# Kernel optimization log

Measured on AMD Instinct MI355X. Metric: run time of the kernel, lower is better.

Reference implementation:

```python
import jax, jax.numpy as jnp
import numpy as np

EPS_LN = 1e-5  # nn.LayerNorm default eps
EPS_AD = 1e-5  # AdaIN calc_mean_std eps


def calc_mean_std(feat):
    # feat: [B, S, D]; instance-norm style stats per channel over the seq axis
    mean = jnp.mean(feat, axis=1, keepdims=True)
    var = jnp.var(feat, axis=1, keepdims=True, ddof=1)  # torch .var() is unbiased
    return mean, jnp.sqrt(var + EPS_AD)


def adain(content, style):
    c_mean, c_std = calc_mean_std(content)
    s_mean, s_std = calc_mean_std(style)
    return (content - c_mean) / c_std * s_std + s_mean


def layernorm(x, g, b):
    mu = jnp.mean(x, axis=-1, keepdims=True)
    var = jnp.mean(jnp.square(x - mu), axis=-1, keepdims=True)
    return (x - mu) * jax.lax.rsqrt(var + EPS_LN) * g + b


def silu(x):
    return x * jax.nn.sigmoid(x)


def setup_inputs() -> dict:
    B, S, D = 64, 256, 1024
    key = jax.random.key(0)
    ks = jax.random.split(key, 8)
    sc = lambda n: 1.0 / np.sqrt(n)
    return {
        "x": jax.random.normal(ks[0], (B, S, 2 * D), jnp.float32),
        "embed": jax.random.normal(ks[1], (B, S, D), jnp.float32),
        "style_code": jax.random.normal(ks[2], (B, S, D), jnp.float32),
        # conct: Linear(2*dim, dim)
        "Wc": jax.random.normal(ks[3], (D, 2 * D), jnp.float32) * sc(2 * D),
        "bc": jnp.zeros((D,), jnp.float32),
        # emb_fc: Linear(dim, dim)
        "We": jax.random.normal(ks[4], (D, D), jnp.float32) * sc(D),
        "be": jnp.zeros((D,), jnp.float32),
        # fc0: Conv1d(seq0, seq1, 1) -> [seq1, seq0] matrix over the seq axis
        "W0": jax.random.normal(ks[5], (S, S), jnp.float32) * sc(S),
        "b0": jnp.zeros((S,), jnp.float32),
        # fc1: Linear(dim, dim)
        "W1": jax.random.normal(ks[6], (D, D), jnp.float32) * sc(D),
        "b1": jnp.zeros((D,), jnp.float32),
        # LayerNorm affine params
        "g0": jnp.ones((D,), jnp.float32),
        "beta0": jnp.zeros((D,), jnp.float32),
        "g1": jnp.ones((D,), jnp.float32),
        "beta1": jnp.zeros((D,), jnp.float32),
    }


def reference(x, embed, style_code, Wc, bc, We, be, W0, b0, W1, b1, g0, beta0, g1, beta1):
    # conct (first=True): [B,S,2D] -> [B,S,D]
    adain_input = jnp.einsum('bse,de->bsd', x, Wc) + bc
    tmp = adain(adain_input, style_code)  # alpha = 1.0 so tmp replaces adain_input
    x = tmp + (jnp.einsum('bsd,ed->bse', silu(embed), We) + be)
    # block 0: LN -> 1x1 Conv1d over seq axis -> SiLU -> residual
    x_ = layernorm(x, g0, beta0)
    x_ = jnp.einsum('ts,bsd->btd', W0, x_) + b0[:, None]
    x = x + silu(x_)
    # block 1: LN -> Linear over dim axis -> SiLU -> residual
    x_ = layernorm(x, g1, beta1)
    x_ = jnp.einsum('bsd,ed->bse', x_, W1) + b1
    x = x + silu(x_)
    return (x, embed, style_code)
```

## Files before the change

kernel.cpp:

```cpp
#include <hip/hip_runtime.h>
#include <cstddef>

#define BB 64
#define SS 256
#define DD 1024
#define MM (BB * SS)

typedef unsigned short u16;
typedef short bf16x8 __attribute__((ext_vector_type(8)));
typedef float f32x4 __attribute__((ext_vector_type(4)));

#define LDSTRIDE 40

__device__ __forceinline__ float silu_f(float v) {
    return v * (1.0f / (1.0f + __expf(-v)));
}

__device__ __forceinline__ void split2(float f0, float f1, unsigned& hp, unsigned& lp) {
    const unsigned b0 = __float_as_uint(f0), b1 = __float_as_uint(f1);
    const unsigned h0 = b0 & 0xFFFF0000u, h1 = b1 & 0xFFFF0000u;
    const float l0 = f0 - __uint_as_float(h0);
    const float l1 = f1 - __uint_as_float(h1);
    hp = (h0 >> 16) | h1;
    lp = (__float_as_uint(l0) >> 16) | (__float_as_uint(l1) & 0xFFFF0000u);
}

template<bool SILU_A, int EPI>
__global__ __launch_bounds__(256, 2)
void gemm_nt_mfma(const float* __restrict__ A, const float* __restrict__ Bw,
                  const float* __restrict__ bias,
                  const float* __restrict__ t0, const float* __restrict__ scl,
                  const float* __restrict__ shf, const float* __restrict__ resid,
                  float* __restrict__ C, int M, int N, int K)
{
    __shared__ u16 lds[4 * 128 * LDSTRIDE];
    u16* Ah = lds;
    u16* Al = lds + 128 * LDSTRIDE;
    u16* Bh = lds + 2 * 128 * LDSTRIDE;
    u16* Bl = lds + 3 * 128 * LDSTRIDE;

    const int nbx = gridDim.x;
    const int nwg = nbx * gridDim.y;
    int lin = blockIdx.y * nbx + blockIdx.x;
    if ((nwg & 7) == 0) {
        const int cpx = nwg >> 3;
        lin = (lin & 7) * cpx + (lin >> 3);
    }
    const int bx = lin % nbx;
    const int by = lin / nbx;
    const int row0 = by * 128;
    const int col0 = bx * 128;

    const int tid  = threadIdx.x;
    const int srow = tid >> 1;
    const int sko  = (tid & 1) << 4;
    const int wbase = srow * LDSTRIDE + sko;

    const float* Ag = A  + (size_t)(row0 + srow) * K + sko;
    const float* Bg = Bw + (size_t)(col0 + srow) * K + sko;

    const int lane = tid & 63;
    const int wid  = tid >> 6;
    const int wr = wid >> 1, wc = wid & 1;
    const int fr = lane & 15;
    const int fh = lane >> 4;
    const int abase = (wr * 64 + fr) * LDSTRIDE + fh * 8;
    const int bbase = (wc * 64 + fr) * LDSTRIDE + fh * 8;

    f32x4 acc[4][4];
    const f32x4 zero = {0.f, 0.f, 0.f, 0.f};
#pragma unroll
    for (int i = 0; i < 4; ++i)
#pragma unroll
        for (int j = 0; j < 4; ++j) acc[i][j] = zero;

    for (int k0 = 0; k0 < K; k0 += 32) {
        float4 va[4], vb[4];
#pragma unroll
        for (int q = 0; q < 4; ++q) va[q] = *(const float4*)(Ag + k0 + q * 4);
#pragma unroll
        for (int q = 0; q < 4; ++q) vb[q] = *(const float4*)(Bg + k0 + q * 4);
        if (SILU_A) {
#pragma unroll
            for (int q = 0; q < 4; ++q) {
                va[q].x = silu_f(va[q].x); va[q].y = silu_f(va[q].y);
                va[q].z = silu_f(va[q].z); va[q].w = silu_f(va[q].w);
            }
        }
        uint4 ah0, al0, ah1, al1, bh0, bl0, bh1, bl1;
        split2(va[0].x, va[0].y, ah0.x, al0.x); split2(va[0].z, va[0].w, ah0.y, al0.y);
        split2(va[1].x, va[1].y, ah0.z, al0.z); split2(va[1].z, va[1].w, ah0.w, al0.w);
        split2(va[2].x, va[2].y, ah1.x, al1.x); split2(va[2].z, va[2].w, ah1.y, al1.y);
        split2(va[3].x, va[3].y, ah1.z, al1.z); split2(va[3].z, va[3].w, ah1.w, al1.w);
        split2(vb[0].x, vb[0].y, bh0.x, bl0.x); split2(vb[0].z, vb[0].w, bh0.y, bl0.y);
        split2(vb[1].x, vb[1].y, bh0.z, bl0.z); split2(vb[1].z, vb[1].w, bh0.w, bl0.w);
        split2(vb[2].x, vb[2].y, bh1.x, bl1.x); split2(vb[2].z, vb[2].w, bh1.y, bl1.y);
        split2(vb[3].x, vb[3].y, bh1.z, bl1.z); split2(vb[3].z, vb[3].w, bh1.w, bl1.w);

        __syncthreads();
        *(uint4*)&Ah[wbase] = ah0;  *(uint4*)&Ah[wbase + 8] = ah1;
        *(uint4*)&Al[wbase] = al0;  *(uint4*)&Al[wbase + 8] = al1;
        *(uint4*)&Bh[wbase] = bh0;  *(uint4*)&Bh[wbase + 8] = bh1;
        *(uint4*)&Bl[wbase] = bl0;  *(uint4*)&Bl[wbase + 8] = bl1;
        __syncthreads();

        bf16x8 fah[4], fal[4];
#pragma unroll
        for (int i = 0; i < 4; ++i) {
            fah[i] = *(const bf16x8*)&Ah[abase + i * 16 * LDSTRIDE];
            fal[i] = *(const bf16x8*)&Al[abase + i * 16 * LDSTRIDE];
        }
#pragma unroll
        for (int j = 0; j < 4; ++j) {
            const bf16x8 fbh = *(const bf16x8*)&Bh[bbase + j * 16 * LDSTRIDE];
            const bf16x8 fbl = *(const bf16x8*)&Bl[bbase + j * 16 * LDSTRIDE];
#pragma unroll
            for (int i = 0; i < 4; ++i) {
                acc[i][j] = __builtin_amdgcn_mfma_f32_16x16x32_bf16(fah[i], fbh, acc[i][j], 0, 0, 0);
                acc[i][j] = __builtin_amdgcn_mfma_f32_16x16x32_bf16(fal[i], fbh, acc[i][j], 0, 0, 0);
                acc[i][j] = __builtin_amdgcn_mfma_f32_16x16x32_bf16(fah[i], fbl, acc[i][j], 0, 0, 0);
            }
        }
    }

#pragma unroll
    for (int i = 0; i < 4; ++i) {
        const int rbase = row0 + wr * 64 + i * 16 + fh * 4;
#pragma unroll
        for (int j = 0; j < 4; ++j) {
            const int c = col0 + wc * 64 + j * 16 + fr;
            const float bsum = bias[c];
            float sc = 0.f, sh = 0.f;
            if (EPI == 1) {
                const int b = rbase >> 8;
                sc = scl[b * DD + c];
                sh = shf[b * DD + c];
            }
#pragma unroll
            for (int r = 0; r < 4; ++r) {
                const int rr = rbase + r;
                const size_t idx = (size_t)rr * N + c;
                const float t = acc[i][j][r] + bsum;
                if (EPI == 0) {
                    C[idx] = t;
                } else if (EPI == 1) {
                    C[idx] = fmaf(t0[idx], sc, sh) + t;
                } else {
                    C[idx] = resid[idx] + silu_f(t);
                }
            }
        }
    }
}

__global__ __launch_bounds__(256)
void gemm_seq(const float* __restrict__ W0, const float* __restrict__ Y,
              const float* __restrict__ bias0, float* __restrict__ X)
{
    __shared__ float As[16][132];
    __shared__ float Bs[16][132];
    const int tid   = threadIdx.x;
    const int batch = blockIdx.z;
    const int row0  = blockIdx.y * 128;
    const int col0  = blockIdx.x * 128;
    const float* Bg = Y + (size_t)batch * SS * DD;
    float* Cb = X + (size_t)batch * SS * DD;
    const int lrA = tid >> 1;
    const int lkA = (tid & 1) * 8;
    const int kB  = tid >> 4;
    const int nB  = (tid & 15) * 8;
    const int ty = tid >> 4;
    const int tx = tid & 15;

    float acc[8][8];
#pragma unroll
    for (int i = 0; i < 8; ++i)
#pragma unroll
        for (int j = 0; j < 8; ++j) acc[i][j] = 0.0f;

    for (int k0 = 0; k0 < SS; k0 += 16) {
        const float* ap = &W0[(size_t)(row0 + lrA) * SS + k0 + lkA];
        float4 a0 = *(const float4*)(ap);
        float4 a1 = *(const float4*)(ap + 4);
        const float* bp = &Bg[(size_t)(k0 + kB) * DD + col0 + nB];
        float4 b0 = *(const float4*)(bp);
        float4 b1 = *(const float4*)(bp + 4);
        As[lkA+0][lrA] = a0.x; As[lkA+1][lrA] = a0.y; As[lkA+2][lrA] = a0.z; As[lkA+3][lrA] = a0.w;
        As[lkA+4][lrA] = a1.x; As[lkA+5][lrA] = a1.y; As[lkA+6][lrA] = a1.z; As[lkA+7][lrA] = a1.w;
        *(float4*)&Bs[kB][nB]     = b0;
        *(float4*)&Bs[kB][nB + 4] = b1;
        __syncthreads();
#pragma unroll
        for (int k = 0; k < 16; ++k) {
            const float4 ra0 = *(const float4*)&As[k][ty * 8];
            const float4 ra1 = *(const float4*)&As[k][ty * 8 + 4];
            const float4 rb0 = *(const float4*)&Bs[k][tx * 8];
            const float4 rb1 = *(const float4*)&Bs[k][tx * 8 + 4];
            const float ra[8] = {ra0.x, ra0.y, ra0.z, ra0.w, ra1.x, ra1.y, ra1.z, ra1.w};
            const float rb[8] = {rb0.x, rb0.y, rb0.z, rb0.w, rb1.x, rb1.y, rb1.z, rb1.w};
#pragma unroll
            for (int i = 0; i < 8; ++i)
#pragma unroll
                for (int j = 0; j < 8; ++j)
                    acc[i][j] = fmaf(ra[i], rb[j], acc[i][j]);
        }
        __syncthreads();
    }

#pragma unroll
    for (int i = 0; i < 8; ++i) {
        const int r = row0 + ty * 8 + i;
        const float bt = bias0[r];
        const size_t rowbase = (size_t)r * DD;
#pragma unroll
        for (int jj = 0; jj < 8; jj += 4) {
            const int c0 = col0 + tx * 8 + jj;
            float4 res = *(const float4*)&Cb[rowbase + c0];
            float4 o;
            o.x = res.x + silu_f(acc[i][jj + 0] + bt);
            o.y = res.y + silu_f(acc[i][jj + 1] + bt);
            o.z = res.z + silu_f(acc[i][jj + 2] + bt);
            o.w = res.w + silu_f(acc[i][jj + 3] + bt);
            *(float4*)&Cb[rowbase + c0] = o;
        }
    }
}

__global__ __launch_bounds__(256)
void adain_stats(const float* __restrict__ t0, const float* __restrict__ style,
                 float* __restrict__ scl, float* __restrict__ shf)
{
    const int idx = blockIdx.x * 256 + threadIdx.x;
    const int b = idx >> 10;
    const int d = idx & (DD - 1);
    const float* pc = t0    + (size_t)b * SS * DD + d;
    const float* ps = style + (size_t)b * SS * DD + d;
    float sc = 0.f, sc2 = 0.f, ss = 0.f, ss2 = 0.f;
    for (int s = 0; s < SS; ++s) {
        const float c  = pc[(size_t)s * DD];
        const float st = ps[(size_t)s * DD];
        sc += c;  sc2 = fmaf(c, c, sc2);
        ss += st; ss2 = fmaf(st, st, ss2);
    }
    const float mc = sc * (1.0f / SS);
    const float ms = ss * (1.0f / SS);
    float vc = (sc2 - (float)SS * mc * mc) * (1.0f / (SS - 1));
    float vs = (ss2 - (float)SS * ms * ms) * (1.0f / (SS - 1));
    vc = fmaxf(vc, 0.f);
    vs = fmaxf(vs, 0.f);
    const float csd = sqrtf(vc + 1e-5f);
    const float ssd = sqrtf(vs + 1e-5f);
    const float sca = ssd / csd;
    scl[idx] = sca;
    shf[idx] = ms - mc * sca;
}

__global__ __launch_bounds__(256)
void ln_rows(const float* __restrict__ X, const float* __restrict__ g,
             const float* __restrict__ beta, float* __restrict__ Y)
{
    const int row  = blockIdx.x * 4 + (threadIdx.x >> 6);
    const int lane = threadIdx.x & 63;
    const float* xr = X + (size_t)row * DD;
    float4 v[4];
    float sum = 0.f, sq = 0.f;
#pragma unroll
    for (int c = 0; c < 4; ++c) {
        v[c] = *(const float4*)&xr[c * 256 + lane * 4];
        sum += v[c].x + v[c].y + v[c].z + v[c].w;
        sq  += v[c].x * v[c].x + v[c].y * v[c].y + v[c].z * v[c].z + v[c].w * v[c].w;
    }
#pragma unroll
    for (int off = 32; off > 0; off >>= 1) {
        sum += __shfl_down(sum, off, 64);
        sq  += __shfl_down(sq,  off, 64);
    }
    sum = __shfl(sum, 0, 64);
    sq  = __shfl(sq,  0, 64);
    const float mu = sum * (1.0f / DD);
    float var = sq * (1.0f / DD) - mu * mu;
    var = fmaxf(var, 0.f);
    const float rs = rsqrtf(var + 1e-5f);
    float* yr = Y + (size_t)row * DD;
#pragma unroll
    for (int c = 0; c < 4; ++c) {
        const int col = c * 256 + lane * 4;
        const float4 gv = *(const float4*)&g[col];
        const float4 bv = *(const float4*)&beta[col];
        float4 o;
        o.x = (v[c].x - mu) * rs * gv.x + bv.x;
        o.y = (v[c].y - mu) * rs * gv.y + bv.y;
        o.z = (v[c].z - mu) * rs * gv.z + bv.z;
        o.w = (v[c].w - mu) * rs * gv.w + bv.w;
        *(float4*)&yr[col] = o;
    }
}

__global__ __launch_bounds__(256)
void copy_pass(const float4* __restrict__ emb, const float4* __restrict__ sty,
               float4* __restrict__ out_emb, float4* __restrict__ out_sty)
{
    const int n4 = MM * DD / 4;
    const int stride = gridDim.x * blockDim.x;
    for (int i = blockIdx.x * blockDim.x + threadIdx.x; i < n4; i += stride) {
        out_emb[i] = emb[i];
        out_sty[i] = sty[i];
    }
}

extern "C" void kernel_launch(void* const* d_in, const int* in_sizes, int n_in,
                              void* d_out, int out_size, void* d_ws, size_t ws_size,
                              hipStream_t stream)
{
    const float* x     = (const float*)d_in[0];
    const float* embed = (const float*)d_in[1];
    const float* style = (const float*)d_in[2];
    const float* Wc    = (const float*)d_in[3];
    const float* bc    = (const float*)d_in[4];
    const float* We    = (const float*)d_in[5];
    const float* be    = (const float*)d_in[6];
    const float* W0    = (const float*)d_in[7];
    const float* b0    = (const float*)d_in[8];
    const float* W1    = (const float*)d_in[9];
    const float* b1    = (const float*)d_in[10];
    const float* g0    = (const float*)d_in[11];
    const float* beta0 = (const float*)d_in[12];
    const float* g1    = (const float*)d_in[13];
    const float* beta1 = (const float*)d_in[14];

    float* out     = (float*)d_out;
    float* out_x   = out;
    float* out_emb = out + (size_t)MM * DD;
    float* out_sty = out + (size_t)2 * MM * DD;

    float* buf0 = out_sty;
    float* buf1 = out_emb;
    float* scl = (float*)d_ws;
    float* shf = scl + BB * DD;

    const dim3 gNT(DD / 128, MM / 128);

    gemm_nt_mfma<false, 0><<<gNT, 256, 0, stream>>>(x, Wc, bc, nullptr, nullptr, nullptr,
                                                    nullptr, buf0, MM, DD, 2 * DD);
    adain_stats<<<BB * DD / 256, 256, 0, stream>>>(buf0, style, scl, shf);
    gemm_nt_mfma<true, 1><<<gNT, 256, 0, stream>>>(embed, We, be, buf0, scl, shf,
                                                   nullptr, buf1, MM, DD, DD);
    ln_rows<<<MM / 4, 256, 0, stream>>>(buf1, g0, beta0, buf0);
    gemm_seq<<<dim3(DD / 128, SS / 128, BB), 256, 0, stream>>>(W0, buf0, b0, buf1);
    ln_rows<<<MM / 4, 256, 0, stream>>>(buf1, g1, beta1, buf0);
    gemm_nt_mfma<false, 2><<<gNT, 256, 0, stream>>>(buf0, W1, b1, nullptr, nullptr, nullptr,
                                                    buf1, out_x, MM, DD, DD);
    copy_pass<<<4096, 256, 0, stream>>>((const float4*)embed, (const float4*)style,
                                        (float4*)out_emb, (float4*)out_sty);
}
```

Measured before the change: 1.067 ms.

## Pre-split operands to bf16 hi/lo, use global_load_lds and MFMA for seq GEMM

Weights and layernorm outputs are split once into swizzled bf16 hi/lo arrays, so the GEMM can stream them straight into LDS with global_load_lds instead of converting fp32 on every tile. The fp32 FMA sequence-axis GEMM is replaced by the same three-pass bf16 MFMA kernel, fed by a transposed LN output, and LDS uses an XOR swizzle in place of padding. LN is split into a stats pass plus a transpose/split pass. This adds several extra kernels and scratch traffic through the output buffers, and the weights are re-split on every call.

After: 988.2 us. -7.4%, faster.

```diff
diff --git a/kernel.cpp b/kernel.cpp
--- a/kernel.cpp
+++ b/kernel.cpp
@@ -1,5 +1,6 @@
 #include <hip/hip_runtime.h>
 #include <cstddef>
+#include <cstdint>
 
 #define BB 64
 #define SS 256
@@ -7,38 +8,89 @@
 #define MM (BB * SS)
 
 typedef unsigned short u16;
+typedef unsigned int u32;
 typedef short bf16x8 __attribute__((ext_vector_type(8)));
 typedef float f32x4 __attribute__((ext_vector_type(4)));
 
-#define LDSTRIDE 40
-
 __device__ __forceinline__ float silu_f(float v) {
     return v * (1.0f / (1.0f + __expf(-v)));
 }
 
-__device__ __forceinline__ void split2(float f0, float f1, unsigned& hp, unsigned& lp) {
-    const unsigned b0 = __float_as_uint(f0), b1 = __float_as_uint(f1);
-    const unsigned h0 = b0 & 0xFFFF0000u, h1 = b1 & 0xFFFF0000u;
-    const float l0 = f0 - __uint_as_float(h0);
-    const float l1 = f1 - __uint_as_float(h1);
-    hp = (h0 >> 16) | h1;
-    lp = (__float_as_uint(l0) >> 16) | (__float_as_uint(l1) & 0xFFFF0000u);
-}
-
-template<bool SILU_A, int EPI>
-__global__ __launch_bounds__(256, 2)
-void gemm_nt_mfma(const float* __restrict__ A, const float* __restrict__ Bw,
-                  const float* __restrict__ bias,
-                  const float* __restrict__ t0, const float* __restrict__ scl,
-                  const float* __restrict__ shf, const float* __restrict__ resid,
-                  float* __restrict__ C, int M, int N, int K)
-{
-    __shared__ u16 lds[4 * 128 * LDSTRIDE];
-    u16* Ah = lds;
-    u16* Al = lds + 128 * LDSTRIDE;
-    u16* Bh = lds + 2 * 128 * LDSTRIDE;
-    u16* Bl = lds + 3 * 128 * LDSTRIDE;
-
+__device__ __forceinline__ int swz4(int r) {
+    return ((r >> 2) & 3) ^ (r & 3);
+}
+
+__device__ __forceinline__ void splitf(float f, u16& h, u16& l) {
+    const u32 b = __float_as_uint(f);
+    const u32 hb = b & 0xFFFF0000u;
+    const float lf = f - __uint_as_float(hb);
+    h = (u16)(hb >> 16);
+    l = (u16)(__float_as_uint(lf) >> 16);
+}
+
+__device__ __forceinline__ void gll16(const void* g, void* l) {
+    __builtin_amdgcn_global_load_lds(
+        (const __attribute__((address_space(1))) u32*)g,
+        (__attribute__((address_space(3))) u32*)l, 16, 0, 0);
+}
+
+__device__ __forceinline__ void cvt16(const float* av, uint4& h0, uint4& h1,
+                                      uint4& l0, uint4& l1) {
+    u16 hh[16], hl[16];
+#pragma unroll
+    for (int m = 0; m < 16; ++m) splitf(av[m], hh[m], hl[m]);
+    u32 ph[8], pl[8];
+#pragma unroll
+    for (int m = 0; m < 8; ++m) {
+        ph[m] = (u32)hh[2 * m] | ((u32)hh[2 * m + 1] << 16);
+        pl[m] = (u32)hl[2 * m] | ((u32)hl[2 * m + 1] << 16);
+    }
+    h0 = make_uint4(ph[0], ph[1], ph[2], ph[3]);
+    h1 = make_uint4(ph[4], ph[5], ph[6], ph[7]);
+    l0 = make_uint4(pl[0], pl[1], pl[2], pl[3]);
+    l1 = make_uint4(pl[4], pl[5], pl[6], pl[7]);
+}
+
+__global__ __launch_bounds__(256)
+void split_w(const float* __restrict__ src, u16* __restrict__ dh,
+             u16* __restrict__ dl, int k8shift)
+{
+    const int idx = blockIdx.x * 256 + threadIdx.x;
+    const int n = idx >> k8shift;
+    const int c = idx & ((1 << k8shift) - 1);
+    const int srcc = (c & ~3) | ((c & 3) ^ swz4(n & 15));
+    const float* sp = src + ((size_t)n << (k8shift + 3)) + srcc * 8;
+    const float4 v0 = *(const float4*)sp;
+    const float4 v1 = *(const float4*)(sp + 4);
+    const float av[8] = {v0.x, v0.y, v0.z, v0.w, v1.x, v1.y, v1.z, v1.w};
+    u16 hh[8], hl[8];
+#pragma unroll
+    for (int m = 0; m < 8; ++m) splitf(av[m], hh[m], hl[m]);
+    u32 ph[4], pl[4];
+#pragma unroll
+    for (int m = 0; m < 4; ++m) {
+        ph[m] = (u32)hh[2 * m] | ((u32)hh[2 * m + 1] << 16);
+        pl[m] = (u32)hl[2 * m] | ((u32)hl[2 * m + 1] << 16);
+    }
+    *(uint4*)&dh[(size_t)idx * 8] = make_uint4(ph[0], ph[1], ph[2], ph[3]);
+    *(uint4*)&dl[(size_t)idx * 8] = make_uint4(pl[0], pl[1], pl[2], pl[3]);
+}
+
+template<int AM, int BM, int EPI>
+__global__ __launch_bounds__(256, (AM == 0 && BM == 0) ? 4 : 3)
+void gemm_bf3(const float* __restrict__ A32,
+              const u16* __restrict__ Ahg, const u16* __restrict__ Alg,
+              const float* __restrict__ B32,
+              const u16* __restrict__ Bhg, const u16* __restrict__ Blg,
+              const float* __restrict__ bias,
+              const float* __restrict__ t0, const float* __restrict__ scl,
+              const float* __restrict__ shf,
+              const float* __restrict__ resid, float* __restrict__ C,
+              int M, int N, int K, long long bsB, long long bsC)
+{
+    __shared__ u16 lds[16384];
+
+    const int z = blockIdx.z;
     const int nbx = gridDim.x;
     const int nwg = nbx * gridDim.y;
     int lin = blockIdx.y * nbx + blockIdx.x;
@@ -48,72 +100,132 @@
     }
     const int bx = lin % nbx;
     const int by = lin / nbx;
-    const int row0 = by * 128;
-    const int col0 = bx * 128;
-
-    const int tid  = threadIdx.x;
+    const int row0 = by * 128, col0 = bx * 128;
+
+    const int tid = threadIdx.x;
+    const int lane = tid & 63, wid = tid >> 6;
+    const int wr = wid >> 1, wc = wid & 1;
+    const int fr = lane & 15, fh = lane >> 4;
+    const int fsw = (fh ^ swz4(fr)) * 8;
+
     const int srow = tid >> 1;
-    const int sko  = (tid & 1) << 4;
-    const int wbase = srow * LDSTRIDE + sko;
-
-    const float* Ag = A  + (size_t)(row0 + srow) * K + sko;
-    const float* Bg = Bw + (size_t)(col0 + srow) * K + sko;
-
-    const int lane = tid & 63;
-    const int wid  = tid >> 6;
-    const int wr = wid >> 1, wc = wid & 1;
-    const int fr = lane & 15;
-    const int fh = lane >> 4;
-    const int abase = (wr * 64 + fr) * LDSTRIDE + fh * 8;
-    const int bbase = (wc * 64 + fr) * LDSTRIDE + fh * 8;
+    const int sko = (tid & 1) << 4;
+    const int ssw = swz4(srow & 15);
+    const int sw0 = srow * 32 + (((sko >> 3) + 0) ^ ssw) * 8;
+    const int sw1 = srow * 32 + (((sko >> 3) + 1) ^ ssw) * 8;
+
+    const float* Ag32 = nullptr;
+    const float* Bg32 = nullptr;
+    if constexpr (AM != 0) Ag32 = A32 + (size_t)(row0 + srow) * K + sko;
+    if constexpr (BM != 0) Bg32 = B32 + (size_t)(col0 + srow) * K + sko;
+
+    const u16* gPre = nullptr; int ldsPre = 0;
+    const u16* gB = nullptr; int ldsB = 0, sib0 = 0;
+
+    if constexpr (AM == 0) {
+        if constexpr (BM == 0) {
+            const u16* gs; int base, lb;
+            if (wid == 0)      { gs = Ahg; base = row0; lb = 0; }
+            else if (wid == 1) { gs = Alg; base = row0; lb = 4096; }
+            else if (wid == 2) { gs = Bhg + (size_t)z * (size_t)bsB; base = col0; lb = 8192; }
+            else               { gs = Blg + (size_t)z * (size_t)bsB; base = col0; lb = 12288; }
+            gPre = gs + (size_t)(base + (lane >> 2)) * K + (lane & 3) * 8;
+            ldsPre = lb;
+        } else {
+            const u16* gs = (wid & 1) ? Alg : Ahg;
+            gPre = gs + (size_t)(row0 + (lane >> 2)) * K + (lane & 3) * 8;
+            ldsPre = (wid & 1) ? 4096 : 0;
+        }
+    } else {
+        gB = ((wid < 2) ? Bhg : Blg) + (size_t)z * (size_t)bsB
+             + (size_t)(col0 + (wid & 1) * 64 + (lane >> 2)) * K + (lane & 3) * 8;
+        ldsB = (wid < 2) ? 8192 : 12288;
+        sib0 = (wid & 1) * 4;
+    }
 
     f32x4 acc[4][4];
-    const f32x4 zero = {0.f, 0.f, 0.f, 0.f};
 #pragma unroll
     for (int i = 0; i < 4; ++i)
 #pragma unroll
-        for (int j = 0; j < 4; ++j) acc[i][j] = zero;
+        for (int j = 0; j < 4; ++j) acc[i][j] = (f32x4){0.f, 0.f, 0.f, 0.f};
 
     for (int k0 = 0; k0 < K; k0 += 32) {
-        float4 va[4], vb[4];
-#pragma unroll
-        for (int q = 0; q < 4; ++q) va[q] = *(const float4*)(Ag + k0 + q * 4);
-#pragma unroll
-        for (int q = 0; q < 4; ++q) vb[q] = *(const float4*)(Bg + k0 + q * 4);
-        if (SILU_A) {
-#pragma unroll
-            for (int q = 0; q < 4; ++q) {
-                va[q].x = silu_f(va[q].x); va[q].y = silu_f(va[q].y);
-                va[q].z = silu_f(va[q].z); va[q].w = silu_f(va[q].w);
+        float av[16], bv[16];
+        if constexpr (AM != 0) {
+            const float4 a0 = *(const float4*)(Ag32 + k0);
+            const float4 a1 = *(const float4*)(Ag32 + k0 + 4);
+            const float4 a2 = *(const float4*)(Ag32 + k0 + 8);
+            const float4 a3 = *(const float4*)(Ag32 + k0 + 12);
+            av[0]=a0.x; av[1]=a0.y; av[2]=a0.z; av[3]=a0.w;
+            av[4]=a1.x; av[5]=a1.y; av[6]=a1.z; av[7]=a1.w;
+            av[8]=a2.x; av[9]=a2.y; av[10]=a2.z; av[11]=a2.w;
+            av[12]=a3.x; av[13]=a3.y; av[14]=a3.z; av[15]=a3.w;
+            if constexpr (AM == 2) {
+#pragma unroll
+                for (int m = 0; m < 16; ++m) av[m] = silu_f(av[m]);
             }
         }
-        uint4 ah0, al0, ah1, al1, bh0, bl0, bh1, bl1;
-        split2(va[0].x, va[0].y, ah0.x, al0.x); split2(va[0].z, va[0].w, ah0.y, al0.y);
-        split2(va[1].x, va[1].y, ah0.z, al0.z); split2(va[1].z, va[1].w, ah0.w, al0.w);
-        split2(va[2].x, va[2].y, ah1.x, al1.x); split2(va[2].z, va[2].w, ah1.y, al1.y);
-        split2(va[3].x, va[3].y, ah1.z, al1.z); split2(va[3].z, va[3].w, ah1.w, al1.w);
-        split2(vb[0].x, vb[0].y, bh0.x, bl0.x); split2(vb[0].z, vb[0].w, bh0.y, bl0.y);
-        split2(vb[1].x, vb[1].y, bh0.z, bl0.z); split2(vb[1].z, vb[1].w, bh0.w, bl0.w);
-        split2(vb[2].x, vb[2].y, bh1.x, bl1.x); split2(vb[2].z, vb[2].w, bh1.y, bl1.y);
-        split2(vb[3].x, vb[3].y, bh1.z, bl1.z); split2(vb[3].z, vb[3].w, bh1.w, bl1.w);
+        if constexpr (BM != 0) {
+            const float4 b0 = *(const float4*)(Bg32 + k0);
+            const float4 b1 = *(const float4*)(Bg32 + k0 + 4);
+            const float4 b2 = *(const float4*)(Bg32 + k0 + 8);
+            const float4 b3 = *(const float4*)(Bg32 + k0 + 12);
+            bv[0]=b0.x; bv[1]=b0.y; bv[2]=b0.z; bv[3]=b0.w;
+            bv[4]=b1.x; bv[5]=b1.y; bv[6]=b1.z; bv[7]=b1.w;
+            bv[8]=b2.x; bv[9]=b2.y; bv[10]=b2.z; bv[11]=b2.w;
+            bv[12]=b3.x; bv[13]=b3.y; bv[14]=b3.z; bv[15]=b3.w;
+        }
 
         __syncthreads();
-        *(uint4*)&Ah[wbase] = ah0;  *(uint4*)&Ah[wbase + 8] = ah1;
-        *(uint4*)&Al[wbase] = al0;  *(uint4*)&Al[wbase + 8] = al1;
-        *(uint4*)&Bh[wbase] = bh0;  *(uint4*)&Bh[wbase + 8] = bh1;
-        *(uint4*)&Bl[wbase] = bl0;  *(uint4*)&Bl[wbase + 8] = bl1;
+
+        if constexpr (AM == 0) {
+            if constexpr (BM == 0) {
+#pragma unroll
+                for (int q = 0; q < 8; ++q)
+                    gll16(gPre + (size_t)q * 16 * K + k0, &lds[ldsPre + q * 512]);
+            } else {
+                if (wid < 2) {
+#pragma unroll
+                    for (int q = 0; q < 8; ++q)
+                        gll16(gPre + (size_t)q * 16 * K + k0, &lds[ldsPre + q * 512]);
+                }
+            }
+        } else {
+#pragma unroll
+            for (int q = 0; q < 4; ++q)
+                gll16(gB + (size_t)q * 16 * K + k0, &lds[ldsB + (sib0 + q) * 512]);
+        }
+
+        if constexpr (AM != 0) {
+            uint4 h0, h1, l0, l1;
+            cvt16(av, h0, h1, l0, l1);
+            *(uint4*)&lds[sw0] = h0;
+            *(uint4*)&lds[sw1] = h1;
+            *(uint4*)&lds[4096 + sw0] = l0;
+            *(uint4*)&lds[4096 + sw1] = l1;
+        }
+        if constexpr (BM != 0) {
+            uint4 h0, h1, l0, l1;
+            cvt16(bv, h0, h1, l0, l1);
+            *(uint4*)&lds[8192 + sw0] = h0;
+            *(uint4*)&lds[8192 + sw1] = h1;
+            *(uint4*)&lds[12288 + sw0] = l0;
+            *(uint4*)&lds[12288 + sw1] = l1;
+        }
         __syncthreads();
 
         bf16x8 fah[4], fal[4];
 #pragma unroll
         for (int i = 0; i < 4; ++i) {
-            fah[i] = *(const bf16x8*)&Ah[abase + i * 16 * LDSTRIDE];
-            fal[i] = *(const bf16x8*)&Al[abase + i * 16 * LDSTRIDE];
+            const int ao = (wr * 64 + i * 16 + fr) * 32 + fsw;
+            fah[i] = *(const bf16x8*)&lds[ao];
+            fal[i] = *(const bf16x8*)&lds[4096 + ao];
         }
 #pragma unroll
         for (int j = 0; j < 4; ++j) {
-            const bf16x8 fbh = *(const bf16x8*)&Bh[bbase + j * 16 * LDSTRIDE];
-            const bf16x8 fbl = *(const bf16x8*)&Bl[bbase + j * 16 * LDSTRIDE];
+            const int bo = (wc * 64 + j * 16 + fr) * 32 + fsw;
+            const bf16x8 fbh = *(const bf16x8*)&lds[8192 + bo];
+            const bf16x8 fbl = *(const bf16x8*)&lds[12288 + bo];
 #pragma unroll
             for (int i = 0; i < 4; ++i) {
                 acc[i][j] = __builtin_amdgcn_mfma_f32_16x16x32_bf16(fah[i], fbh, acc[i][j], 0, 0, 0);
@@ -123,15 +235,16 @@
         }
     }
 
+    const size_t cz = (size_t)z * (size_t)bsC;
 #pragma unroll
     for (int i = 0; i < 4; ++i) {
         const int rbase = row0 + wr * 64 + i * 16 + fh * 4;
 #pragma unroll
         for (int j = 0; j < 4; ++j) {
             const int c = col0 + wc * 64 + j * 16 + fr;
-            const float bsum = bias[c];
-            float sc = 0.f, sh = 0.f;
-            if (EPI == 1) {
+            float bcol = 0.f, sc = 0.f, sh = 0.f;
+            if constexpr (EPI != 3) bcol = bias[c];
+            if constexpr (EPI == 1) {
                 const int b = rbase >> 8;
                 sc = scl[b * DD + c];
                 sh = shf[b * DD + c];
@@ -139,89 +252,12 @@
 #pragma unroll
             for (int r = 0; r < 4; ++r) {
                 const int rr = rbase + r;
-                const size_t idx = (size_t)rr * N + c;
-                const float t = acc[i][j][r] + bsum;
-                if (EPI == 0) {
-                    C[idx] = t;
-                } else if (EPI == 1) {
-                    C[idx] = fmaf(t0[idx], sc, sh) + t;
-                } else {
-                    C[idx] = resid[idx] + silu_f(t);
-                }
+                const size_t idx = cz + (size_t)rr * N + c;
+                const float t = acc[i][j][r] + ((EPI == 3) ? bias[rr] : bcol);
+                if constexpr (EPI == 0) C[idx] = t;
+                else if constexpr (EPI == 1) C[idx] = fmaf(t0[idx], sc, sh) + t;
+                else C[idx] = resid[idx] + silu_f(t);
             }
-        }
-    }
-}
-
-__global__ __launch_bounds__(256)
-void gemm_seq(const float* __restrict__ W0, const float* __restrict__ Y,
-              const float* __restrict__ bias0, float* __restrict__ X)
-{
-    __shared__ float As[16][132];
-    __shared__ float Bs[16][132];
-    const int tid   = threadIdx.x;
-    const int batch = blockIdx.z;
-    const int row0  = blockIdx.y * 128;
-    const int col0  = blockIdx.x * 128;
-    const float* Bg = Y + (size_t)batch * SS * DD;
-    float* Cb = X + (size_t)batch * SS * DD;
-    const int lrA = tid >> 1;
-    const int lkA = (tid & 1) * 8;
-    const int kB  = tid >> 4;
-    const int nB  = (tid & 15) * 8;
-    const int ty = tid >> 4;
-    const int tx = tid & 15;
-
-    float acc[8][8];
-#pragma unroll
-    for (int i = 0; i < 8; ++i)
-#pragma unroll
-        for (int j = 0; j < 8; ++j) acc[i][j] = 0.0f;
-
-    for (int k0 = 0; k0 < SS; k0 += 16) {
-        const float* ap = &W0[(size_t)(row0 + lrA) * SS + k0 + lkA];
-        float4 a0 = *(const float4*)(ap);
-        float4 a1 = *(const float4*)(ap + 4);
-        const float* bp = &Bg[(size_t)(k0 + kB) * DD + col0 + nB];
-        float4 b0 = *(const float4*)(bp);
-        float4 b1 = *(const float4*)(bp + 4);
-        As[lkA+0][lrA] = a0.x; As[lkA+1][lrA] = a0.y; As[lkA+2][lrA] = a0.z; As[lkA+3][lrA] = a0.w;
-        As[lkA+4][lrA] = a1.x; As[lkA+5][lrA] = a1.y; As[lkA+6][lrA] = a1.z; As[lkA+7][lrA] = a1.w;
-        *(float4*)&Bs[kB][nB]     = b0;
-        *(float4*)&Bs[kB][nB + 4] = b1;
-        __syncthreads();
-#pragma unroll
-        for (int k = 0; k < 16; ++k) {
-            const float4 ra0 = *(const float4*)&As[k][ty * 8];
-            const float4 ra1 = *(const float4*)&As[k][ty * 8 + 4];
-            const float4 rb0 = *(const float4*)&Bs[k][tx * 8];
-            const float4 rb1 = *(const float4*)&Bs[k][tx * 8 + 4];
-            const float ra[8] = {ra0.x, ra0.y, ra0.z, ra0.w, ra1.x, ra1.y, ra1.z, ra1.w};
-            const float rb[8] = {rb0.x, rb0.y, rb0.z, rb0.w, rb1.x, rb1.y, rb1.z, rb1.w};
-#pragma unroll
-            for (int i = 0; i < 8; ++i)
-#pragma unroll
-                for (int j = 0; j < 8; ++j)
-                    acc[i][j] = fmaf(ra[i], rb[j], acc[i][j]);
-        }
-        __syncthreads();
-    }
-
-#pragma unroll
-    for (int i = 0; i < 8; ++i) {
-        const int r = row0 + ty * 8 + i;
-        const float bt = bias0[r];
-        const size_t rowbase = (size_t)r * DD;
-#pragma unroll
-        for (int jj = 0; jj < 8; jj += 4) {
-            const int c0 = col0 + tx * 8 + jj;
-            float4 res = *(const float4*)&Cb[rowbase + c0];
-            float4 o;
-            o.x = res.x + silu_f(acc[i][jj + 0] + bt);
-            o.y = res.y + silu_f(acc[i][jj + 1] + bt);
-            o.z = res.z + silu_f(acc[i][jj + 2] + bt);
-            o.w = res.w + silu_f(acc[i][jj + 3] + bt);
-            *(float4*)&Cb[rowbase + c0] = o;
         }
     }
 }
@@ -256,19 +292,98 @@
 }
 
 __global__ __launch_bounds__(256)
-void ln_rows(const float* __restrict__ X, const float* __restrict__ g,
-             const float* __restrict__ beta, float* __restrict__ Y)
-{
-    const int row  = blockIdx.x * 4 + (threadIdx.x >> 6);
+void ln_stats(const float* __restrict__ X, float* __restrict__ mu, float* __restrict__ rs)
+{
+    const int row = blockIdx.x * 4 + (threadIdx.x >> 6);
+    const int lane = threadIdx.x & 63;
+    const float* xr = X + (size_t)row * DD;
+    float sum = 0.f, sq = 0.f;
+#pragma unroll
+    for (int c = 0; c < 4; ++c) {
+        const float4 v = *(const float4*)&xr[c * 256 + lane * 4];
+        sum += v.x + v.y + v.z + v.w;
+        sq += v.x * v.x + v.y * v.y + v.z * v.z + v.w * v.w;
+    }
+#pragma unroll
+    for (int off = 32; off > 0; off >>= 1) {
+        sum += __shfl_down(sum, off, 64);
+        sq  += __shfl_down(sq,  off, 64);
+    }
+    if (lane == 0) {
+        const float m = sum * (1.0f / DD);
+        float var = sq * (1.0f / DD) - m * m;
+        var = fmaxf(var, 0.f);
+        mu[row] = m;
+        rs[row] = rsqrtf(var + 1e-5f);
+    }
+}
+
+__global__ __launch_bounds__(256)
+void ln_t_split(const float* __restrict__ X, const float* __restrict__ mu,
+                const float* __restrict__ rs, const float* __restrict__ g,
+                const float* __restrict__ beta,
+                u16* __restrict__ yTh, u16* __restrict__ yTl)
+{
+    __shared__ u16 th[64 * 66];
+    __shared__ u16 tl[64 * 66];
+    const int b = blockIdx.z;
+    const int s0 = blockIdx.y * 64;
+    const int d0 = blockIdx.x * 64;
+    const int t = threadIdx.x;
+    const int sl0 = t >> 4;
+    const int dl4 = (t & 15) * 4;
+    const float4 gv = *(const float4*)&g[d0 + dl4];
+    const float4 bv = *(const float4*)&beta[d0 + dl4];
+#pragma unroll
+    for (int q = 0; q < 4; ++q) {
+        const int s_local = q * 16 + sl0;
+        const int row = b * SS + s0 + s_local;
+        const float4 v = *(const float4*)&X[(size_t)row * DD + d0 + dl4];
+        const float m = mu[row], r = rs[row];
+        const float vals[4] = {(v.x - m) * r * gv.x + bv.x, (v.y - m) * r * gv.y + bv.y,
+                               (v.z - m) * r * gv.z + bv.z, (v.w - m) * r * gv.w + bv.w};
+#pragma unroll
+        for (int j = 0; j < 4; ++j) {
+            u16 hh, lo;
+            splitf(vals[j], hh, lo);
+            th[(dl4 + j) * 66 + s_local] = hh;
+            tl[(dl4 + j) * 66 + s_local] = lo;
+        }
+    }
+    __syncthreads();
+    const int dl = t >> 2;
+    const int sc = (t & 3) * 16;
+    u32 ah[8], al[8];
+#pragma unroll
+    for (int jj = 0; jj < 8; ++jj) {
+        ah[jj] = *(const u32*)&th[dl * 66 + sc + jj * 2];
+        al[jj] = *(const u32*)&tl[dl * 66 + sc + jj * 2];
+    }
+    const int cc0 = (s0 + sc) >> 3;
+    const int swv = swz4(dl & 15);
+    const int p0 = (cc0 & ~3) | ((cc0 & 3) ^ swv);
+    const int p1 = (cc0 & ~3) | ((((cc0 & 3) + 1)) ^ swv);
+    const size_t rb = ((size_t)b * DD + d0 + dl) * SS;
+    *(uint4*)&yTh[rb + p0 * 8] = make_uint4(ah[0], ah[1], ah[2], ah[3]);
+    *(uint4*)&yTh[rb + p1 * 8] = make_uint4(ah[4], ah[5], ah[6], ah[7]);
+    *(uint4*)&yTl[rb + p0 * 8] = make_uint4(al[0], al[1], al[2], al[3]);
+    *(uint4*)&yTl[rb + p1 * 8] = make_uint4(al[4], al[5], al[6], al[7]);
+}
+
+__global__ __launch_bounds__(256)
+void ln_split(const float* __restrict__ X, const float* __restrict__ g,
+              const float* __restrict__ beta, u16* __restrict__ zh, u16* __restrict__ zl)
+{
+    const int row = blockIdx.x * 4 + (threadIdx.x >> 6);
     const int lane = threadIdx.x & 63;
     const float* xr = X + (size_t)row * DD;
     float4 v[4];
     float sum = 0.f, sq = 0.f;
 #pragma unroll
-    for (int c = 0; c < 4; ++c) {
-        v[c] = *(const float4*)&xr[c * 256 + lane * 4];
-        sum += v[c].x + v[c].y + v[c].z + v[c].w;
-        sq  += v[c].x * v[c].x + v[c].y * v[c].y + v[c].z * v[c].z + v[c].w * v[c].w;
+    for (int q = 0; q < 4; ++q) {
+        v[q] = *(const float4*)&xr[lane * 16 + q * 4];
+        sum += v[q].x + v[q].y + v[q].z + v[q].w;
+        sq += v[q].x * v[q].x + v[q].y * v[q].y + v[q].z * v[q].z + v[q].w * v[q].w;
     }
 #pragma unroll
     for (int off = 32; off > 0; off >>= 1) {
@@ -277,23 +392,32 @@
     }
     sum = __shfl(sum, 0, 64);
     sq  = __shfl(sq,  0, 64);
-    const float mu = sum * (1.0f / DD);
-    float var = sq * (1.0f / DD) - mu * mu;
+    const float m = sum * (1.0f / DD);
+    float var = sq * (1.0f / DD) - m * m;
     var = fmaxf(var, 0.f);
-    const float rs = rsqrtf(var + 1e-5f);
-    float* yr = Y + (size_t)row * DD;
-#pragma unroll
-    for (int c = 0; c < 4; ++c) {
-        const int col = c * 256 + lane * 4;
-        const float4 gv = *(const float4*)&g[col];
-        const float4 bv = *(const float4*)&beta[col];
-        float4 o;
-        o.x = (v[c].x - mu) * rs * gv.x + bv.x;
-        o.y = (v[c].y - mu) * rs * gv.y + bv.y;
-        o.z = (v[c].z - mu) * rs * gv.z + bv.z;
-        o.w = (v[c].w - mu) * rs * gv.w + bv.w;
-        *(float4*)&yr[col] = o;
-    }
+    const float r = rsqrtf(var + 1e-5f);
+    float ov[16];
+#pragma unroll
+    for (int q = 0; q < 4; ++q) {
+        const float4 gq = *(const float4*)&g[lane * 16 + q * 4];
+        const float4 bq = *(const float4*)&beta[lane * 16 + q * 4];
+        ov[q * 4 + 0] = (v[q].x - m) * r * gq.x + bq.x;
+        ov[q * 4 + 1] = (v[q].y - m) * r * gq.y + bq.y;
+        ov[q * 4 + 2] = (v[q].z - m) * r * gq.z + bq.z;
+        ov[q * 4 + 3] = (v[q].w - m) * r * gq.w + bq.w;
+    }
+    uint4 h0, h1, l0, l1;
+    cvt16(ov, h0, h1, l0, l1);
+    const int swr = swz4(row & 15);
+    const int c0 = lane * 2;
+    const int p0 = (c0 & ~3) | ((c0 & 3) ^ swr);
+    const int p1 = ((c0 + 1) & ~3) | (((c0 + 1) & 3) ^ swr);
+    u16* zr = zh + (size_t)row * DD;
+    u16* zr2 = zl + (size_t)row * DD;
+    *(uint4*)&zr[p0 * 8]  = h0;
+    *(uint4*)&zr[p1 * 8]  = h1;
+    *(uint4*)&zr2[p0 * 8] = l0;
+    *(uint4*)&zr2[p1 * 8] = l1;
 }
 
 __global__ __launch_bounds__(256)
@@ -335,21 +459,45 @@
 
     float* buf0 = out_sty;
     float* buf1 = out_emb;
-    float* scl = (float*)d_ws;
+
+    u16* Wch = (u16*)out_x;
+    u16* Wcl = Wch + 2097152;
+    u16* Weh = Wcl + 2097152;
+    u16* Wel = Weh + 1048576;
+    u16* W0h = Wel + 1048576;
+    u16* W0l = W0h + 65536;
+    float* scl = (float*)(W0l + 65536);
     float* shf = scl + BB * DD;
-
-    const dim3 gNT(DD / 128, MM / 128);
-
-    gemm_nt_mfma<false, 0><<<gNT, 256, 0, stream>>>(x, Wc, bc, nullptr, nullptr, nullptr,
-                                                    nullptr, buf0, MM, DD, 2 * DD);
+    float* muv = shf + BB * DD;
+    float* rsv = muv + MM;
+
+    u16* yTh = (u16*)buf0;
+    u16* yTl = yTh + (size_t)MM * DD;
+    u16* zh  = (u16*)buf0;
+    u16* zl  = zh + (size_t)MM * DD;
+
+    const dim3 gNT(DD / 128, MM / 128, 1);
+
+    split_w<<<1024, 256, 0, stream>>>(Wc, Wch, Wcl, 8);
+    split_w<<<512, 256, 0, stream>>>(We, Weh, Wel, 7);
+    split_w<<<32, 256, 0, stream>>>(W0, W0h, W0l, 5);
+
+    gemm_bf3<1, 0, 0><<<gNT, 256, 0, stream>>>(
+        x, nullptr, nullptr, nullptr, Wch, Wcl, bc, nullptr, nullptr, nullptr,
+        nullptr, buf0, MM, DD, 2 * DD, 0, 0);
     adain_stats<<<BB * DD / 256, 256, 0, stream>>>(buf0, style, scl, shf);
-    gemm_nt_mfma<true, 1><<<gNT, 256, 0, stream>>>(embed, We, be, buf0, scl, shf,
-                                                   nullptr, buf1, MM, DD, DD);
-    ln_rows<<<MM / 4, 256, 0, stream>>>(buf1, g0, beta0, buf0);
-    gemm_seq<<<dim3(DD / 128, SS / 128, BB), 256, 0, stream>>>(W0, buf0, b0, buf1);
-    ln_rows<<<MM / 4, 256, 0, stream>>>(buf1, g1, beta1, buf0);
-    gemm_nt_mfma<false, 2><<<gNT, 256, 0, stream>>>(buf0, W1, b1, nullptr, nullptr, nullptr,
-                                                    buf1, out_x, MM, DD, DD);
+    gemm_bf3<2, 0, 1><<<gNT, 256, 0, stream>>>(
+        embed, nullptr, nullptr, nullptr, Weh, Wel, be, buf0, scl, shf,
+        nullptr, buf1, MM, DD, DD, 0, 0);
+    ln_stats<<<MM / 4, 256, 0, stream>>>(buf1, muv, rsv);
+    ln_t_split<<<dim3(16, 4, 64), 256, 0, stream>>>(buf1, muv, rsv, g0, beta0, yTh, yTl);
+    gemm_bf3<0, 0, 3><<<dim3(8, 2, 64), 256, 0, stream>>>(
+        nullptr, W0h, W0l, nullptr, yTh, yTl, b0, nullptr, nullptr, nullptr,
+        buf1, buf1, SS, DD, SS, 262144LL, 262144LL);
+    ln_split<<<MM / 4, 256, 0, stream>>>(buf1, g1, beta1, zh, zl);
+    gemm_bf3<0, 1, 2><<<gNT, 256, 0, stream>>>(
+        nullptr, zh, zl, W1, nullptr, nullptr, b1, nullptr, nullptr, nullptr,
+        buf1, out_x, MM, DD, DD, 0, 0);
     copy_pass<<<4096, 256, 0, stream>>>((const float4*)embed, (const float4*)style,
                                         (float4*)out_emb, (float4*)out_sty);
 }
```
